# Optimization experiments

Measured on AMD Instinct MI355X. Metric: run time of the kernel, lower is better.

## Reference

```python
import jax, jax.numpy as jnp
import numpy as np

STATE_DIM, HIDDEN, GRU_H = 128, 64, 64
B, T = 2048, 512


def setup_inputs() -> dict:
    key = jax.random.key(0)
    ks = jax.random.split(key, 9)
    s = lambda fan_in: 1.0 / np.sqrt(fan_in)
    return {
        "state_seq": jax.random.normal(ks[0], (B, T, STATE_DIM), dtype=jnp.float32),
        "W1": jax.random.uniform(ks[1], (HIDDEN, STATE_DIM), minval=-s(STATE_DIM), maxval=s(STATE_DIM)),
        "b1": jax.random.uniform(ks[2], (HIDDEN,), minval=-s(STATE_DIM), maxval=s(STATE_DIM)),
        "W_ih": jax.random.uniform(ks[3], (3 * GRU_H, HIDDEN), minval=-s(GRU_H), maxval=s(GRU_H)),
        "W_hh": jax.random.uniform(ks[4], (3 * GRU_H, GRU_H), minval=-s(GRU_H), maxval=s(GRU_H)),
        "b_ih": jax.random.uniform(ks[5], (3 * GRU_H,), minval=-s(GRU_H), maxval=s(GRU_H)),
        "b_hh": jax.random.uniform(ks[6], (3 * GRU_H,), minval=-s(GRU_H), maxval=s(GRU_H)),
        "W_out": jax.random.uniform(ks[7], (1, GRU_H), minval=-s(GRU_H), maxval=s(GRU_H)),
        "b_out": jax.random.uniform(ks[8], (1,), minval=-s(GRU_H), maxval=s(GRU_H)),
    }


def reference(state_seq, W1, b1, W_ih, W_hh, b_ih, b_hh, W_out, b_out):
    H = W_hh.shape[1]
    # input projection + ReLU: [B, T, HIDDEN]
    x = jax.nn.relu(jnp.einsum("btd,hd->bth", state_seq, W1) + b1)
    # precompute input-side gate activations for all timesteps: [T, B, 3H]
    gx = (jnp.einsum("bth,gh->btg", x, W_ih) + b_ih).transpose(1, 0, 2)

    def step(h, gx_t):
        gh = h @ W_hh.T + b_hh  # [B, 3H]
        r = jax.nn.sigmoid(gx_t[:, :H] + gh[:, :H])
        z = jax.nn.sigmoid(gx_t[:, H:2 * H] + gh[:, H:2 * H])
        n = jnp.tanh(gx_t[:, 2 * H:] + r * gh[:, 2 * H:])
        h_new = (1.0 - z) * n + z * h
        return h_new, None

    h0 = jnp.zeros((state_seq.shape[0], H), dtype=state_seq.dtype)
    h_final, _ = jax.lax.scan(step, h0, gx)
    value = h_final @ W_out.T + b_out  # [B, 1]
    return value
```

## Files before the change

### kernel.cpp

```cpp
#include <hip/hip_runtime.h>
#include <cstdint>
#include <cstddef>


#define T_STEPS 512
#define SD 128
#define HID 64
#define NB 16

typedef __attribute__((ext_vector_type(8))) short short8;
typedef __attribute__((ext_vector_type(4))) float floatx4;

__device__ __forceinline__ unsigned short f2bf(float f) {
  union { float f; unsigned u; } v; v.f = f;
  return (unsigned short)((v.u + 0x7FFFu + ((v.u >> 16) & 1u)) >> 16);
}

__device__ __forceinline__ short8 pack8(float4 a, float4 b) {
  short8 v;
  v[0] = (short)f2bf(a.x); v[1] = (short)f2bf(a.y);
  v[2] = (short)f2bf(a.z); v[3] = (short)f2bf(a.w);
  v[4] = (short)f2bf(b.x); v[5] = (short)f2bf(b.y);
  v[6] = (short)f2bf(b.z); v[7] = (short)f2bf(b.w);
  return v;
}


__global__ __launch_bounds__(256) void gru_fused(
    const float* __restrict__ S,
    const float* __restrict__ W1,
    const float* __restrict__ b1,
    const float* __restrict__ Wih,
    const float* __restrict__ Whh,
    const float* __restrict__ bih,
    const float* __restrict__ bhh,
    const float* __restrict__ Wout,
    const float* __restrict__ bout,
    float* __restrict__ out)
{
  __shared__ __attribute__((aligned(16))) short sS[4 * 64 * 8];
  __shared__ __attribute__((aligned(16))) short sX[2 * 64 * 8];
  __shared__ __attribute__((aligned(16))) short sHb[2 * 64 * 8];
  __shared__ float sHf[NB * 68];

  const int td = threadIdx.x;
  const int w = td >> 6;
  const int lane = td & 63;
  const int l16 = lane & 15;
  const int quad = lane >> 4;
  const int r0 = blockIdx.x * NB;

  short8 w1f[4], wihf[3][2], whhf[3][2];
  {
    const float* p = W1 + (16 * w + l16) * SD + quad * 8;
#pragma unroll
    for (int c = 0; c < 4; ++c) {
      short8 f;
#pragma unroll
      for (int j = 0; j < 8; ++j) f[j] = (short)f2bf(p[32 * c + j]);
      w1f[c] = f;
    }
  }
#pragma unroll
  for (int i = 0; i < 3; ++i) {
    const int n = 16 * (w + 4 * i) + l16;
#pragma unroll
    for (int c = 0; c < 2; ++c) {
      const float* q  = Wih + n * HID + 32 * c + quad * 8;
      const float* q2 = Whh + n * HID + 32 * c + quad * 8;
      short8 f, g;
#pragma unroll
      for (int j = 0; j < 8; ++j) {
        f[j] = (short)f2bf(q[j]);
        g[j] = (short)f2bf(q2[j]);
      }
      wihf[i][c] = f;
      whhf[i][c] = g;
    }
  }
  const int col = 16 * w + l16;
  const float b1c = b1[col];
  float bihc[3], bhhc[3];
#pragma unroll
  for (int i = 0; i < 3; ++i) {
    bihc[i] = bih[col + 64 * i];
    bhhc[i] = bhh[col + 64 * i];
  }

  const int sm = td & 15;
  const int k0 = (td >> 4) * 8;
  const float* sp = S + ((size_t)(r0 + sm) * T_STEPS) * SD + k0;
  short* sSslot = &sS[(((k0 >> 5) * 64) + ((k0 >> 3) & 3) * 16 + sm) * 8];

  for (int i = td; i < 2 * 64 * 8; i += 256) sHb[i] = 0;
  for (int i = td; i < NB * 68; i += 256) sHf[i] = 0.0f;

  float4 pf0 = *(const float4*)(sp);
  float4 pf1 = *(const float4*)(sp + 4);
  *(short8*)sSslot = pack8(pf0, pf1);
  pf0 = *(const float4*)(sp + 1 * SD);
  pf1 = *(const float4*)(sp + 1 * SD + 4);
  __syncthreads();

  const int mbase = quad * 4;
  const int pc = col >> 5, pqk = (col >> 3) & 3, pj = col & 7;
  short* xWp  = &sX [((pc * 64) + pqk * 16 + mbase) * 8 + pj];
  short* hbWp = &sHb[((pc * 64) + pqk * 16 + mbase) * 8 + pj];
  float* hfp  = &sHf[mbase * 68 + col];

  for (int t = 0; t < T_STEPS; ++t) {
    short8 hf0 = *(const short8*)&sHb[(0 * 64 + lane) * 8];
    short8 hf1 = *(const short8*)&sHb[(1 * 64 + lane) * 8];
    short8 sf[4];
#pragma unroll
    for (int c = 0; c < 4; ++c) sf[c] = *(const short8*)&sS[(c * 64 + lane) * 8];

    floatx4 accGH[3];
#pragma unroll
    for (int i = 0; i < 3; ++i) {
      floatx4 a = { bhhc[i], bhhc[i], bhhc[i], bhhc[i] };
      a = __builtin_amdgcn_mfma_f32_16x16x32_bf16(hf0, whhf[i][0], a, 0, 0, 0);
      a = __builtin_amdgcn_mfma_f32_16x16x32_bf16(hf1, whhf[i][1], a, 0, 0, 0);
      accGH[i] = a;
    }
    floatx4 accX = { b1c, b1c, b1c, b1c };
#pragma unroll
    for (int c = 0; c < 4; ++c)
      accX = __builtin_amdgcn_mfma_f32_16x16x32_bf16(sf[c], w1f[c], accX, 0, 0, 0);

#pragma unroll
    for (int r = 0; r < 4; ++r) {
      float xv = accX[r];
      xv = xv > 0.0f ? xv : 0.0f;
      xWp[r * 8] = (short)f2bf(xv);
    }
    __syncthreads();

    if (t + 1 < T_STEPS) *(short8*)sSslot = pack8(pf0, pf1);
    {
      const int tn = (t + 2 < T_STEPS) ? t + 2 : T_STEPS - 1;
      pf0 = *(const float4*)(sp + (size_t)tn * SD);
      pf1 = *(const float4*)(sp + (size_t)tn * SD + 4);
    }

    short8 xf0 = *(const short8*)&sX[(0 * 64 + lane) * 8];
    short8 xf1 = *(const short8*)&sX[(1 * 64 + lane) * 8];
    floatx4 accGX[3];
#pragma unroll
    for (int i = 0; i < 3; ++i) {
      floatx4 a = { bihc[i], bihc[i], bihc[i], bihc[i] };
      a = __builtin_amdgcn_mfma_f32_16x16x32_bf16(xf0, wihf[i][0], a, 0, 0, 0);
      a = __builtin_amdgcn_mfma_f32_16x16x32_bf16(xf1, wihf[i][1], a, 0, 0, 0);
      accGX[i] = a;
    }
#pragma unroll
    for (int r = 0; r < 4; ++r) {
      float gr = accGX[0][r] + accGH[0][r];
      float gz = accGX[1][r] + accGH[1][r];
      float rg = 1.0f / (1.0f + __expf(-gr));
      float zg = 1.0f / (1.0f + __expf(-gz));
      float gn = accGX[2][r] + rg * accGH[2][r];
      float ng = 2.0f / (1.0f + __expf(-2.0f * gn)) - 1.0f;
      float ho = hfp[r * 68];
      float hn = zg * (ho - ng) + ng;
      hfp[r * 68] = hn;
      hbWp[r * 8] = (short)f2bf(hn);
    }
    __syncthreads();
  }

  if (td < NB) {
    float acc = bout[0];
#pragma unroll
    for (int c = 0; c < HID; ++c) acc += sHf[td * 68 + c] * Wout[c];
    out[r0 + td] = acc;
  }
}

extern "C" void kernel_launch(void* const* d_in, const int* in_sizes, int n_in,
                              void* d_out, int out_size, void* d_ws, size_t ws_size,
                              hipStream_t stream) {
  const float* S    = (const float*)d_in[0];
  const float* W1   = (const float*)d_in[1];
  const float* b1   = (const float*)d_in[2];
  const float* Wih  = (const float*)d_in[3];
  const float* Whh  = (const float*)d_in[4];
  const float* bih  = (const float*)d_in[5];
  const float* bhh  = (const float*)d_in[6];
  const float* Wout = (const float*)d_in[7];
  const float* bout = (const float*)d_in[8];
  float* out = (float*)d_out;

  const int B = in_sizes[0] / (T_STEPS * SD);
  dim3 grid(B / NB);
  gru_fused<<<grid, 256, 0, stream>>>(S, W1, b1, Wih, Whh, bih, bhh, Wout, bout, out);
}
```

Before: 1.043 ms.

## Split GRU kernel into producer and consumer warps with double-buffered stages

The block grows to 512 threads. Four producer waves compute the input projection and the input-side gate preactivations one or two steps ahead and write them into double-buffered shared memory. Four consumer waves run only the recurrent matmul and the gate math, which shortens the serial critical path and leaves one barrier per step. The hidden state now lives in registers, the output reduction uses shared atomics, and the activations use rcp intrinsics. The cost is more shared memory and threads per block, which may lower occupancy, and extra pipeline-fill logic.

New measurement: 913.1 us. 1.14x faster.

```diff
diff --git a/kernel.cpp b/kernel.cpp
--- a/kernel.cpp
+++ b/kernel.cpp
@@ -25,8 +25,15 @@
   return v;
 }
 
-
-__global__ __launch_bounds__(256) void gru_fused(
+__device__ __forceinline__ float sigm(float x) {
+  return __builtin_amdgcn_rcpf(1.0f + __expf(-x));
+}
+
+__device__ __forceinline__ int apack(int m, int k) {
+  return ((k >> 5) * 64 + ((k >> 3) & 3) * 16 + m) * 8 + (k & 7);
+}
+
+__global__ __launch_bounds__(512, 2) void gru_pc(
     const float* __restrict__ S,
     const float* __restrict__ W1,
     const float* __restrict__ b1,
@@ -38,10 +45,11 @@
     const float* __restrict__ bout,
     float* __restrict__ out)
 {
-  __shared__ __attribute__((aligned(16))) short sS[4 * 64 * 8];
-  __shared__ __attribute__((aligned(16))) short sX[2 * 64 * 8];
-  __shared__ __attribute__((aligned(16))) short sHb[2 * 64 * 8];
-  __shared__ float sHf[NB * 68];
+  __shared__ __attribute__((aligned(16))) short sS[2][4 * 64 * 8];
+  __shared__ __attribute__((aligned(16))) short sX[2][2 * 64 * 8];
+  __shared__ __attribute__((aligned(16))) short sHb[2][2 * 64 * 8];
+  __shared__ __attribute__((aligned(16))) float gGX[2][3][4][64 * 4];
+  __shared__ float sOut[NB];
 
   const int td = threadIdx.x;
   const int w = td >> 6;
@@ -49,132 +57,195 @@
   const int l16 = lane & 15;
   const int quad = lane >> 4;
   const int r0 = blockIdx.x * NB;
-
-  short8 w1f[4], wihf[3][2], whhf[3][2];
-  {
-    const float* p = W1 + (16 * w + l16) * SD + quad * 8;
-#pragma unroll
-    for (int c = 0; c < 4; ++c) {
-      short8 f;
-#pragma unroll
-      for (int j = 0; j < 8; ++j) f[j] = (short)f2bf(p[32 * c + j]);
-      w1f[c] = f;
-    }
-  }
-#pragma unroll
-  for (int i = 0; i < 3; ++i) {
-    const int n = 16 * (w + 4 * i) + l16;
-#pragma unroll
-    for (int c = 0; c < 2; ++c) {
-      const float* q  = Wih + n * HID + 32 * c + quad * 8;
-      const float* q2 = Whh + n * HID + 32 * c + quad * 8;
-      short8 f, g;
-#pragma unroll
-      for (int j = 0; j < 8; ++j) {
-        f[j] = (short)f2bf(q[j]);
-        g[j] = (short)f2bf(q2[j]);
-      }
-      wihf[i][c] = f;
-      whhf[i][c] = g;
-    }
-  }
-  const int col = 16 * w + l16;
-  const float b1c = b1[col];
-  float bihc[3], bhhc[3];
-#pragma unroll
-  for (int i = 0; i < 3; ++i) {
-    bihc[i] = bih[col + 64 * i];
-    bhhc[i] = bhh[col + 64 * i];
-  }
-
-  const int sm = td & 15;
-  const int k0 = (td >> 4) * 8;
+  const bool consumer = (w < 4);
+
+  short8 whhf[3][2];
+  float bhhc[3];
+  float ho[4] = {0.0f, 0.0f, 0.0f, 0.0f};
+  const int ccol = 16 * (w & 3) + l16;
+  short* hwBase[2];
+  hwBase[0] = &sHb[0][apack(quad * 4, ccol)];
+  hwBase[1] = &sHb[1][apack(quad * 4, ccol)];
+
+  const int wp = w & 3;
+  short8 w1f[4], wihf[3][2];
+  float b1c = 0.0f, bihc[3];
+  const int pt = td & 255;
+  const int sm = pt & 15;
+  const int k0 = (pt >> 4) * 8;
   const float* sp = S + ((size_t)(r0 + sm) * T_STEPS) * SD + k0;
-  short* sSslot = &sS[(((k0 >> 5) * 64) + ((k0 >> 3) & 3) * 16 + sm) * 8];
-
-  for (int i = td; i < 2 * 64 * 8; i += 256) sHb[i] = 0;
-  for (int i = td; i < NB * 68; i += 256) sHf[i] = 0.0f;
-
-  float4 pf0 = *(const float4*)(sp);
-  float4 pf1 = *(const float4*)(sp + 4);
-  *(short8*)sSslot = pack8(pf0, pf1);
-  pf0 = *(const float4*)(sp + 1 * SD);
-  pf1 = *(const float4*)(sp + 1 * SD + 4);
-  __syncthreads();
-
-  const int mbase = quad * 4;
-  const int pc = col >> 5, pqk = (col >> 3) & 3, pj = col & 7;
-  short* xWp  = &sX [((pc * 64) + pqk * 16 + mbase) * 8 + pj];
-  short* hbWp = &sHb[((pc * 64) + pqk * 16 + mbase) * 8 + pj];
-  float* hfp  = &sHf[mbase * 68 + col];
+  const int sSoff = apack(sm, k0);
+  const int pcol = 16 * wp + l16;
+  short* xwBase[2];
+  xwBase[0] = &sX[0][apack(quad * 4, pcol)];
+  xwBase[1] = &sX[1][apack(quad * 4, pcol)];
+  float4 pf0, pf1;
+
+  if (consumer) {
+#pragma unroll
+    for (int i = 0; i < 3; ++i) {
+      const int n = 16 * (wp + 4 * i) + l16;
+#pragma unroll
+      for (int c = 0; c < 2; ++c) {
+        const float* q = Whh + n * HID + 32 * c + quad * 8;
+        short8 g;
+#pragma unroll
+        for (int j = 0; j < 8; ++j) g[j] = (short)f2bf(q[j]);
+        whhf[i][c] = g;
+      }
+      bhhc[i] = bhh[ccol + 64 * i];
+    }
+    for (int i = td; i < 2 * 64 * 8; i += 256) sHb[0][i] = 0;
+    if (td < NB) sOut[td] = 0.0f;
+  } else {
+    {
+      const float* p = W1 + pcol * SD + quad * 8;
+#pragma unroll
+      for (int c = 0; c < 4; ++c) {
+        short8 f;
+#pragma unroll
+        for (int j = 0; j < 8; ++j) f[j] = (short)f2bf(p[32 * c + j]);
+        w1f[c] = f;
+      }
+      b1c = b1[pcol];
+    }
+#pragma unroll
+    for (int i = 0; i < 3; ++i) {
+      const int n = 16 * (wp + 4 * i) + l16;
+#pragma unroll
+      for (int c = 0; c < 2; ++c) {
+        const float* q = Wih + n * HID + 32 * c + quad * 8;
+        short8 f;
+#pragma unroll
+        for (int j = 0; j < 8; ++j) f[j] = (short)f2bf(q[j]);
+        wihf[i][c] = f;
+      }
+      bihc[i] = bih[pcol + 64 * i];
+    }
+    float4 a0 = *(const float4*)(sp);
+    float4 a1 = *(const float4*)(sp + 4);
+    float4 c0 = *(const float4*)(sp + SD);
+    float4 c1 = *(const float4*)(sp + SD + 4);
+    *(short8*)&sS[0][sSoff] = pack8(a0, a1);
+    *(short8*)&sS[1][sSoff] = pack8(c0, c1);
+    pf0 = *(const float4*)(sp + 2 * SD);
+    pf1 = *(const float4*)(sp + 2 * SD + 4);
+  }
+  __syncthreads();
+
+  if (!consumer) {
+#pragma unroll
+    for (int s = 0; s < 2; ++s) {
+      short8 sf[4];
+#pragma unroll
+      for (int c = 0; c < 4; ++c) sf[c] = *(const short8*)&sS[s][(c * 64 + lane) * 8];
+      floatx4 ax = {b1c, b1c, b1c, b1c};
+      floatx4 ax2 = {0.0f, 0.0f, 0.0f, 0.0f};
+      ax  = __builtin_amdgcn_mfma_f32_16x16x32_bf16(sf[0], w1f[0], ax, 0, 0, 0);
+      ax  = __builtin_amdgcn_mfma_f32_16x16x32_bf16(sf[1], w1f[1], ax, 0, 0, 0);
+      ax2 = __builtin_amdgcn_mfma_f32_16x16x32_bf16(sf[2], w1f[2], ax2, 0, 0, 0);
+      ax2 = __builtin_amdgcn_mfma_f32_16x16x32_bf16(sf[3], w1f[3], ax2, 0, 0, 0);
+#pragma unroll
+      for (int r = 0; r < 4; ++r) {
+        float xv = ax[r] + ax2[r];
+        xwBase[s][r * 8] = (short)f2bf(xv > 0.0f ? xv : 0.0f);
+      }
+    }
+  }
+  __syncthreads();
+
+  if (!consumer) {
+    short8 xf0 = *(const short8*)&sX[0][(0 * 64 + lane) * 8];
+    short8 xf1 = *(const short8*)&sX[0][(1 * 64 + lane) * 8];
+#pragma unroll
+    for (int i = 0; i < 3; ++i) {
+      floatx4 a = {bihc[i], bihc[i], bihc[i], bihc[i]};
+      a = __builtin_amdgcn_mfma_f32_16x16x32_bf16(xf0, wihf[i][0], a, 0, 0, 0);
+      a = __builtin_amdgcn_mfma_f32_16x16x32_bf16(xf1, wihf[i][1], a, 0, 0, 0);
+      *(floatx4*)&gGX[0][i][wp][lane * 4] = a;
+    }
+    *(short8*)&sS[0][sSoff] = pack8(pf0, pf1);
+    pf0 = *(const float4*)(sp + (size_t)3 * SD);
+    pf1 = *(const float4*)(sp + (size_t)3 * SD + 4);
+  }
+  __syncthreads();
 
   for (int t = 0; t < T_STEPS; ++t) {
-    short8 hf0 = *(const short8*)&sHb[(0 * 64 + lane) * 8];
-    short8 hf1 = *(const short8*)&sHb[(1 * 64 + lane) * 8];
-    short8 sf[4];
-#pragma unroll
-    for (int c = 0; c < 4; ++c) sf[c] = *(const short8*)&sS[(c * 64 + lane) * 8];
-
-    floatx4 accGH[3];
-#pragma unroll
-    for (int i = 0; i < 3; ++i) {
-      floatx4 a = { bhhc[i], bhhc[i], bhhc[i], bhhc[i] };
-      a = __builtin_amdgcn_mfma_f32_16x16x32_bf16(hf0, whhf[i][0], a, 0, 0, 0);
-      a = __builtin_amdgcn_mfma_f32_16x16x32_bf16(hf1, whhf[i][1], a, 0, 0, 0);
-      accGH[i] = a;
-    }
-    floatx4 accX = { b1c, b1c, b1c, b1c };
-#pragma unroll
-    for (int c = 0; c < 4; ++c)
-      accX = __builtin_amdgcn_mfma_f32_16x16x32_bf16(sf[c], w1f[c], accX, 0, 0, 0);
-
-#pragma unroll
-    for (int r = 0; r < 4; ++r) {
-      float xv = accX[r];
-      xv = xv > 0.0f ? xv : 0.0f;
-      xWp[r * 8] = (short)f2bf(xv);
-    }
-    __syncthreads();
-
-    if (t + 1 < T_STEPS) *(short8*)sSslot = pack8(pf0, pf1);
-    {
-      const int tn = (t + 2 < T_STEPS) ? t + 2 : T_STEPS - 1;
+    if (consumer) {
+      const int pH = t & 1;
+      floatx4 gx0 = *(const floatx4*)&gGX[pH][0][wp][lane * 4];
+      floatx4 gx1 = *(const floatx4*)&gGX[pH][1][wp][lane * 4];
+      floatx4 gx2 = *(const floatx4*)&gGX[pH][2][wp][lane * 4];
+      short8 hf0 = *(const short8*)&sHb[pH][(0 * 64 + lane) * 8];
+      short8 hf1 = *(const short8*)&sHb[pH][(1 * 64 + lane) * 8];
+      floatx4 g0 = {bhhc[0], bhhc[0], bhhc[0], bhhc[0]};
+      floatx4 g1 = {bhhc[1], bhhc[1], bhhc[1], bhhc[1]};
+      floatx4 g2 = {bhhc[2], bhhc[2], bhhc[2], bhhc[2]};
+      g0 = __builtin_amdgcn_mfma_f32_16x16x32_bf16(hf0, whhf[0][0], g0, 0, 0, 0);
+      g1 = __builtin_amdgcn_mfma_f32_16x16x32_bf16(hf0, whhf[1][0], g1, 0, 0, 0);
+      g2 = __builtin_amdgcn_mfma_f32_16x16x32_bf16(hf0, whhf[2][0], g2, 0, 0, 0);
+      g0 = __builtin_amdgcn_mfma_f32_16x16x32_bf16(hf1, whhf[0][1], g0, 0, 0, 0);
+      g1 = __builtin_amdgcn_mfma_f32_16x16x32_bf16(hf1, whhf[1][1], g1, 0, 0, 0);
+      g2 = __builtin_amdgcn_mfma_f32_16x16x32_bf16(hf1, whhf[2][1], g2, 0, 0, 0);
+      short* hw = hwBase[1 - pH];
+#pragma unroll
+      for (int r = 0; r < 4; ++r) {
+        float rg = sigm(gx0[r] + g0[r]);
+        float zg = sigm(gx1[r] + g1[r]);
+        float gn = gx2[r] + rg * g2[r];
+        float e = __expf(2.0f * gn);
+        float ng = 1.0f - 2.0f * __builtin_amdgcn_rcpf(e + 1.0f);
+        float hn = zg * (ho[r] - ng) + ng;
+        ho[r] = hn;
+        hw[r * 8] = (short)f2bf(hn);
+      }
+    } else {
+      const int pGX = (t + 1) & 1;
+      const int pXr = (t + 1) & 1;
+      const int pXw = t & 1;
+      const int pSr = t & 1;
+      const int pSw = (t + 1) & 1;
+
+      short8 xf0 = *(const short8*)&sX[pXr][(0 * 64 + lane) * 8];
+      short8 xf1 = *(const short8*)&sX[pXr][(1 * 64 + lane) * 8];
+      short8 sf[4];
+#pragma unroll
+      for (int c = 0; c < 4; ++c) sf[c] = *(const short8*)&sS[pSr][(c * 64 + lane) * 8];
+
+#pragma unroll
+      for (int i = 0; i < 3; ++i) {
+        floatx4 a = {bihc[i], bihc[i], bihc[i], bihc[i]};
+        a = __builtin_amdgcn_mfma_f32_16x16x32_bf16(xf0, wihf[i][0], a, 0, 0, 0);
+        a = __builtin_amdgcn_mfma_f32_16x16x32_bf16(xf1, wihf[i][1], a, 0, 0, 0);
+        *(floatx4*)&gGX[pGX][i][wp][lane * 4] = a;
+      }
+      floatx4 ax = {b1c, b1c, b1c, b1c};
+      floatx4 ax2 = {0.0f, 0.0f, 0.0f, 0.0f};
+      ax  = __builtin_amdgcn_mfma_f32_16x16x32_bf16(sf[0], w1f[0], ax, 0, 0, 0);
+      ax  = __builtin_amdgcn_mfma_f32_16x16x32_bf16(sf[1], w1f[1], ax, 0, 0, 0);
+      ax2 = __builtin_amdgcn_mfma_f32_16x16x32_bf16(sf[2], w1f[2], ax2, 0, 0, 0);
+      ax2 = __builtin_amdgcn_mfma_f32_16x16x32_bf16(sf[3], w1f[3], ax2, 0, 0, 0);
+      short* xw = xwBase[pXw];
+#pragma unroll
+      for (int r = 0; r < 4; ++r) {
+        float xv = ax[r] + ax2[r];
+        xw[r * 8] = (short)f2bf(xv > 0.0f ? xv : 0.0f);
+      }
+      *(short8*)&sS[pSw][sSoff] = pack8(pf0, pf1);
+      int tn = t + 4; if (tn > T_STEPS - 1) tn = T_STEPS - 1;
       pf0 = *(const float4*)(sp + (size_t)tn * SD);
       pf1 = *(const float4*)(sp + (size_t)tn * SD + 4);
     }
-
-    short8 xf0 = *(const short8*)&sX[(0 * 64 + lane) * 8];
-    short8 xf1 = *(const short8*)&sX[(1 * 64 + lane) * 8];
-    floatx4 accGX[3];
-#pragma unroll
-    for (int i = 0; i < 3; ++i) {
-      floatx4 a = { bihc[i], bihc[i], bihc[i], bihc[i] };
-      a = __builtin_amdgcn_mfma_f32_16x16x32_bf16(xf0, wihf[i][0], a, 0, 0, 0);
-      a = __builtin_amdgcn_mfma_f32_16x16x32_bf16(xf1, wihf[i][1], a, 0, 0, 0);
-      accGX[i] = a;
-    }
-#pragma unroll
-    for (int r = 0; r < 4; ++r) {
-      float gr = accGX[0][r] + accGH[0][r];
-      float gz = accGX[1][r] + accGH[1][r];
-      float rg = 1.0f / (1.0f + __expf(-gr));
-      float zg = 1.0f / (1.0f + __expf(-gz));
-      float gn = accGX[2][r] + rg * accGH[2][r];
-      float ng = 2.0f / (1.0f + __expf(-2.0f * gn)) - 1.0f;
-      float ho = hfp[r * 68];
-      float hn = zg * (ho - ng) + ng;
-      hfp[r * 68] = hn;
-      hbWp[r * 8] = (short)f2bf(hn);
-    }
     __syncthreads();
   }
 
-  if (td < NB) {
-    float acc = bout[0];
-#pragma unroll
-    for (int c = 0; c < HID; ++c) acc += sHf[td * 68 + c] * Wout[c];
-    out[r0 + td] = acc;
-  }
+  if (consumer) {
+#pragma unroll
+    for (int r = 0; r < 4; ++r)
+      atomicAdd(&sOut[quad * 4 + r], ho[r] * Wout[ccol]);
+  }
+  __syncthreads();
+  if (td < NB) out[r0 + td] = sOut[td] + bout[0];
 }
 
 extern "C" void kernel_launch(void* const* d_in, const int* in_sizes, int n_in,
@@ -193,5 +264,5 @@
 
   const int B = in_sizes[0] / (T_STEPS * SD);
   dim3 grid(B / NB);
-  gru_fused<<<grid, 256, 0, stream>>>(S, W1, b1, Wih, Whh, bih, bhh, Wout, bout, out);
-}
+  gru_pc<<<grid, 512, 0, stream>>>(S, W1, b1, Wih, Whh, bih, bhh, Wout, bout, out);
+}
```
